# Kernel tuning notes

Hardware: AMD Instinct MI355X
Metric: run time of the kernel (lower is better)

Reference implementation:

```python
import jax, jax.numpy as jnp
import numpy as np

N_NODES = 50000
N_EDGES = 800000
NODE_DIM = 128
IN_CH = 64
OUT_CH = 16
N_GRAPHS = 512
N_LAYERS = 5
BN_EPS = 1e-5


def setup_inputs() -> dict:
    key = jax.random.key(0)
    ks = jax.random.split(key, 16)
    s = lambda fan_in: 1.0 / np.sqrt(fan_in)
    inp = {
        "x": jax.random.normal(ks[0], (N_NODES, NODE_DIM), dtype=jnp.float32),
        "edge_index": jax.random.randint(ks[1], (2, N_EDGES), 0, N_NODES, dtype=jnp.int64),
        "batch": jnp.sort(jax.random.randint(ks[2], (N_NODES,), 0, N_GRAPHS, dtype=jnp.int64)),
        "enc_W": jax.random.normal(ks[3], (NODE_DIM, IN_CH), dtype=jnp.float32) * s(NODE_DIM),
        "enc_b": jnp.zeros((IN_CH,), dtype=jnp.float32),
        "conv_W1": jax.random.normal(ks[4], (N_LAYERS, IN_CH, IN_CH), dtype=jnp.float32) * s(IN_CH),
        "conv_b1": jnp.zeros((N_LAYERS, IN_CH), dtype=jnp.float32),
        "conv_W2": jax.random.normal(ks[5], (N_LAYERS, IN_CH, IN_CH), dtype=jnp.float32) * s(IN_CH),
        "conv_b2": jnp.zeros((N_LAYERS, IN_CH), dtype=jnp.float32),
        "bn_gamma": jnp.ones((N_LAYERS, IN_CH), dtype=jnp.float32),
        "bn_beta": jnp.zeros((N_LAYERS, IN_CH), dtype=jnp.float32),
        "fc1_W": jax.random.normal(ks[6], (IN_CH, IN_CH), dtype=jnp.float32) * s(IN_CH),
        "fc1_b": jnp.zeros((IN_CH,), dtype=jnp.float32),
        "fc2_W": jax.random.normal(ks[7], (IN_CH, OUT_CH), dtype=jnp.float32) * s(IN_CH),
        "fc2_b": jnp.zeros((OUT_CH,), dtype=jnp.float32),
    }
    return inp


def reference(x, edge_index, batch, enc_W, enc_b, conv_W1, conv_b1, conv_W2,
              conv_b2, bn_gamma, bn_beta, fc1_W, fc1_b, fc2_W, fc2_b):
    src, dst = edge_index[0], edge_index[1]
    # node feature encoder
    h = x @ enc_W + enc_b  # [N, C]
    for l in range(N_LAYERS):
        # GINConv (eps=0): (1+eps)*x + sum_{j->i} x_j, then 2-layer MLP
        agg = jax.ops.segment_sum(h[src], dst, num_segments=N_NODES)
        z = h + agg
        z = jax.nn.relu(z @ conv_W1[l] + conv_b1[l]) @ conv_W2[l] + conv_b2[l]
        z = jax.nn.relu(z)
        # BatchNorm1d (training stats, biased variance)
        mean = jnp.mean(z, axis=0)
        var = jnp.mean(jnp.square(z - mean), axis=0)
        h = (z - mean) * jax.lax.rsqrt(var + BN_EPS) * bn_gamma[l] + bn_beta[l]
    # global add pool over graphs
    g = jax.ops.segment_sum(h, batch, num_segments=N_GRAPHS)  # [G, C]
    g = jax.nn.relu(g @ fc1_W + fc1_b)
    # dropout is identity in eval mode
    out = g @ fc2_W + fc2_b  # [G, OUT_CH]
    return out
```

## Files before the change

kernel.cpp:

```cpp
#include <hip/hip_runtime.h>
#include <hip/hip_fp16.h>

#define N_NODES 50000
#define N_EDGES 800000
#define NODE_DIM 128
#define C 64
#define N_GRAPHS 512
#define N_LAYERS 5
#define BN_EPS 1e-5f

#define SCAN_BLOCKS 196
#define NBUCK 196
#define ECHUNK 4096

typedef unsigned int u32;

__device__ inline float2 h2f(u32 v) {
    __half2 h; __builtin_memcpy(&h, &v, 4);
    return __half22float2(h);
}
__device__ inline u32 f2h2(float a, float b) {
    __half2 h = __floats2half2_rn(a, b);
    u32 v; __builtin_memcpy(&v, &h, 4);
    return v;
}

__global__ __launch_bounds__(256) void enc_kernel(const float* __restrict__ x,
                                                  const float* __restrict__ W,
                                                  const float* __restrict__ b,
                                                  u32* __restrict__ z) {
    __shared__ float As[64 * 132];
    __shared__ float Ws[NODE_DIM * C];
    int t = threadIdx.x;
    int tc = t & 15, tr = t >> 4;
    for (int i = t; i < NODE_DIM * C; i += 256) Ws[i] = W[i];
    int row0 = blockIdx.x * 128;
    float4 bv = ((const float4*)b)[tc];
    float acc[8][4];
#pragma unroll
    for (int i = 0; i < 8; ++i) { acc[i][0] = bv.x; acc[i][1] = bv.y; acc[i][2] = bv.z; acc[i][3] = bv.w; }

    for (int kc = 0; kc < 2; ++kc) {
        __syncthreads();
        for (int it = 0; it < 8; ++it) {
            int idx = t + 256 * it;
            int r = idx >> 4, f4 = idx & 15;
            int grow = row0 + r;
            float4 v = (grow < N_NODES) ? ((const float4*)x)[grow * 32 + kc * 16 + f4]
                                        : make_float4(0.f, 0.f, 0.f, 0.f);
            int k4 = f4 * 4;
            As[(k4 + 0) * 132 + r] = v.x;
            As[(k4 + 1) * 132 + r] = v.y;
            As[(k4 + 2) * 132 + r] = v.z;
            As[(k4 + 3) * 132 + r] = v.w;
        }
        __syncthreads();
#pragma unroll 4
        for (int k = 0; k < 64; ++k) {
            const float* ap = As + k * 132 + tr * 8;
            float4 a0 = *(const float4*)(ap);
            float4 a1 = *(const float4*)(ap + 4);
            float4 w = *(const float4*)(Ws + (kc * 64 + k) * C + tc * 4);
            float av[8] = {a0.x, a0.y, a0.z, a0.w, a1.x, a1.y, a1.z, a1.w};
#pragma unroll
            for (int i = 0; i < 8; ++i) {
                acc[i][0] = fmaf(av[i], w.x, acc[i][0]);
                acc[i][1] = fmaf(av[i], w.y, acc[i][1]);
                acc[i][2] = fmaf(av[i], w.z, acc[i][2]);
                acc[i][3] = fmaf(av[i], w.w, acc[i][3]);
            }
        }
    }
#pragma unroll
    for (int i = 0; i < 8; ++i) {
        int grow = row0 + tr * 8 + i;
        if (grow < N_NODES) {
            uint2 o;
            o.x = f2h2(acc[i][0], acc[i][1]);
            o.y = f2h2(acc[i][2], acc[i][3]);
            ((uint2*)z)[grow * 16 + tc] = o;
        }
    }
}

__global__ __launch_bounds__(256) void csr_hist(const int* __restrict__ ei,
                                                int* __restrict__ bcount) {
    __shared__ int lhist[NBUCK];
    int t = threadIdx.x;
    if (t < NBUCK) lhist[t] = 0;
    __syncthreads();
    int e0 = blockIdx.x * ECHUNK;
    int e1 = min(e0 + ECHUNK, N_EDGES);
    for (int e = e0 + t; e < e1; e += 256)
        atomicAdd(&lhist[ei[N_EDGES + e] >> 8], 1);
    __syncthreads();
    if (t < NBUCK && lhist[t] > 0) atomicAdd(&bcount[t], lhist[t]);
}

__global__ __launch_bounds__(256) void csr_bscan(const int* __restrict__ bcount,
                                                 int* __restrict__ bbase,
                                                 int* __restrict__ bcursor,
                                                 int* __restrict__ offs) {
    __shared__ int s[256];
    int t = threadIdx.x;
    int v = (t < NBUCK) ? bcount[t] : 0;
    s[t] = v;
    for (int off = 1; off < 256; off <<= 1) {
        __syncthreads();
        int x = (t >= off) ? s[t - off] : 0;
        __syncthreads();
        s[t] += x;
    }
    __syncthreads();
    if (t < NBUCK) {
        bbase[t + 1] = s[t];
        bcursor[t] = s[t] - v;
    }
    if (t == 0) { bbase[0] = 0; offs[N_NODES] = N_EDGES; }
}

__global__ __launch_bounds__(256) void csr_stage(const int* __restrict__ ei,
                                                 int* __restrict__ bcursor,
                                                 u32* __restrict__ staged) {
    __shared__ int lhist[NBUCK];
    __shared__ int lbase[NBUCK];
    __shared__ int lcur[NBUCK];
    int t = threadIdx.x;
    if (t < NBUCK) lhist[t] = 0;
    __syncthreads();
    int e0 = blockIdx.x * ECHUNK;
    int e1 = min(e0 + ECHUNK, N_EDGES);
    for (int e = e0 + t; e < e1; e += 256)
        atomicAdd(&lhist[ei[N_EDGES + e] >> 8], 1);
    __syncthreads();
    if (t < NBUCK) {
        int c = lhist[t];
        lbase[t] = (c > 0) ? atomicAdd(&bcursor[t], c) : 0;
        lcur[t] = 0;
    }
    __syncthreads();
    for (int e = e0 + t; e < e1; e += 256) {
        int src = ei[e];
        int dst = ei[N_EDGES + e];
        int bk = dst >> 8;
        int r = atomicAdd(&lcur[bk], 1);
        staged[lbase[bk] + r] = (u32)src | ((u32)(dst & 255) << 16);
    }
}

__global__ __launch_bounds__(256) void csr_finalize(const u32* __restrict__ staged,
                                                    const int* __restrict__ bbase,
                                                    int* __restrict__ csr,
                                                    int* __restrict__ offs) {
    __shared__ int lhist[256];
    __shared__ int lexc[256];
    __shared__ int lcur[256];
    int t = threadIdx.x;
    int b = blockIdx.x;
    int sbeg = bbase[b], send = bbase[b + 1];
    lhist[t] = 0;
    __syncthreads();
    for (int i = sbeg + t; i < send; i += 256)
        atomicAdd(&lhist[(staged[i] >> 16) & 255], 1);
    __syncthreads();
    int v = lhist[t];
    lexc[t] = v;
    for (int off = 1; off < 256; off <<= 1) {
        __syncthreads();
        int x = (t >= off) ? lexc[t - off] : 0;
        __syncthreads();
        lexc[t] += x;
    }
    __syncthreads();
    int excl = lexc[t] - v;
    int node = b * 256 + t;
    if (node < N_NODES) offs[node] = sbeg + excl;
    lcur[t] = excl;
    __syncthreads();
    for (int i = sbeg + t; i < send; i += 256) {
        u32 ent = staged[i];
        int dlow = (ent >> 16) & 255;
        int r = atomicAdd(&lcur[dlow], 1);
        csr[sbeg + r] = (int)(ent & 0xFFFFu);
    }
}

__global__ __launch_bounds__(256) void gstart_kernel(const int* __restrict__ batch,
                                                     int* __restrict__ goffs) {
    int n = blockIdx.x * 256 + threadIdx.x;
    if (n >= N_NODES) return;
    if (n == 0) {
        for (int g = 0; g <= batch[0]; ++g) goffs[g] = 0;
    } else {
        int bp = batch[n - 1], bc = batch[n];
        for (int g = bp + 1; g <= bc; ++g) goffs[g] = n;
    }
    if (n == N_NODES - 1) {
        for (int g = batch[n] + 1; g <= N_GRAPHS; ++g) goffs[g] = N_NODES;
    }
}

__global__ __launch_bounds__(256) void mlp_gather_kernel(const int* __restrict__ csr_src,
                                                         const int* __restrict__ offs,
                                                         const u32* __restrict__ z_in,
                                                         const float* __restrict__ ss,
                                                         int use_ss,
                                                         u32* __restrict__ z_out,
                                                         const float* __restrict__ W1,
                                                         const float* __restrict__ b1,
                                                         const float* __restrict__ W2,
                                                         const float* __restrict__ b2,
                                                         float* __restrict__ stats) {
    __shared__ float As[64 * 68];
    __shared__ float Ws[C * C];
    int t = threadIdx.x;
    int tc = t & 15, tr = t >> 4;
    for (int i = t; i < C * C; i += 256) Ws[i] = W1[i];
    int row0 = blockIdx.x * 64;

    float4 sc = make_float4(1.f, 1.f, 1.f, 1.f);
    float4 sh = make_float4(0.f, 0.f, 0.f, 0.f);
    if (use_ss) {
        sc = ((const float4*)ss)[tc];
        sh = ((const float4*)(ss + C))[tc];
    }

    const uint2* z2 = (const uint2*)z_in;
    for (int it = 0; it < 4; ++it) {
        int r = tr + 16 * it;
        int node = row0 + r;
        float4 acc = make_float4(0.f, 0.f, 0.f, 0.f);
        if (node < N_NODES) {
            uint2 sv = z2[node * 16 + tc];
            float2 f0 = h2f(sv.x), f1 = h2f(sv.y);
            acc.x = f0.x; acc.y = f0.y; acc.z = f1.x; acc.w = f1.y;
            int beg = offs[node], end = offs[node + 1];
            int e = beg;
            for (; e + 3 < end; e += 4) {
                int s0 = csr_src[e], s1 = csr_src[e + 1], s2 = csr_src[e + 2], s3 = csr_src[e + 3];
                uint2 v0 = z2[s0 * 16 + tc], v1 = z2[s1 * 16 + tc];
                uint2 v2 = z2[s2 * 16 + tc], v3 = z2[s3 * 16 + tc];
                float2 a0 = h2f(v0.x), a1 = h2f(v1.x), a2 = h2f(v2.x), a3 = h2f(v3.x);
                float2 c0 = h2f(v0.y), c1 = h2f(v1.y), c2 = h2f(v2.y), c3 = h2f(v3.y);
                acc.x += (a0.x + a1.x) + (a2.x + a3.x);
                acc.y += (a0.y + a1.y) + (a2.y + a3.y);
                acc.z += (c0.x + c1.x) + (c2.x + c3.x);
                acc.w += (c0.y + c1.y) + (c2.y + c3.y);
            }
            for (; e < end; ++e) {
                uint2 v = z2[csr_src[e] * 16 + tc];
                float2 a = h2f(v.x), c = h2f(v.y);
                acc.x += a.x; acc.y += a.y; acc.z += c.x; acc.w += c.y;
            }
            float cnt = (float)(end - beg + 1);
            acc.x = fmaf(acc.x, sc.x, cnt * sh.x);
            acc.y = fmaf(acc.y, sc.y, cnt * sh.y);
            acc.z = fmaf(acc.z, sc.z, cnt * sh.z);
            acc.w = fmaf(acc.w, sc.w, cnt * sh.w);
        }
        int k4 = tc * 4;
        As[(k4 + 0) * 68 + r] = acc.x;
        As[(k4 + 1) * 68 + r] = acc.y;
        As[(k4 + 2) * 68 + r] = acc.z;
        As[(k4 + 3) * 68 + r] = acc.w;
    }
    __syncthreads();

    float4 b1v = ((const float4*)b1)[tc];
    float a[4][4];
#pragma unroll
    for (int i = 0; i < 4; ++i) { a[i][0] = b1v.x; a[i][1] = b1v.y; a[i][2] = b1v.z; a[i][3] = b1v.w; }
#pragma unroll 4
    for (int k = 0; k < 64; ++k) {
        float4 av = *(const float4*)(As + k * 68 + tr * 4);
        float4 w = *(const float4*)(Ws + k * C + tc * 4);
        float avv[4] = {av.x, av.y, av.z, av.w};
#pragma unroll
        for (int i = 0; i < 4; ++i) {
            a[i][0] = fmaf(avv[i], w.x, a[i][0]);
            a[i][1] = fmaf(avv[i], w.y, a[i][1]);
            a[i][2] = fmaf(avv[i], w.z, a[i][2]);
            a[i][3] = fmaf(avv[i], w.w, a[i][3]);
        }
    }
    __syncthreads();

#pragma unroll
    for (int i = 0; i < 4; ++i)
#pragma unroll
        for (int j = 0; j < 4; ++j)
            As[(tc * 4 + j) * 68 + tr * 4 + i] = fmaxf(a[i][j], 0.f);
    for (int i = t; i < C * C; i += 256) Ws[i] = W2[i];
    __syncthreads();

    float4 b2v = ((const float4*)b2)[tc];
#pragma unroll
    for (int i = 0; i < 4; ++i) { a[i][0] = b2v.x; a[i][1] = b2v.y; a[i][2] = b2v.z; a[i][3] = b2v.w; }
#pragma unroll 4
    for (int k = 0; k < 64; ++k) {
        float4 av = *(const float4*)(As + k * 68 + tr * 4);
        float4 w = *(const float4*)(Ws + k * C + tc * 4);
        float avv[4] = {av.x, av.y, av.z, av.w};
#pragma unroll
        for (int i = 0; i < 4; ++i) {
            a[i][0] = fmaf(avv[i], w.x, a[i][0]);
            a[i][1] = fmaf(avv[i], w.y, a[i][1]);
            a[i][2] = fmaf(avv[i], w.z, a[i][2]);
            a[i][3] = fmaf(avv[i], w.w, a[i][3]);
        }
    }

    float lsum[4] = {0.f, 0.f, 0.f, 0.f};
    float lsq[4] = {0.f, 0.f, 0.f, 0.f};
#pragma unroll
    for (int i = 0; i < 4; ++i) {
        int grow = row0 + tr * 4 + i;
        if (grow < N_NODES) {
            float o0 = fmaxf(a[i][0], 0.f), o1 = fmaxf(a[i][1], 0.f);
            float o2 = fmaxf(a[i][2], 0.f), o3 = fmaxf(a[i][3], 0.f);
            uint2 o;
            o.x = f2h2(o0, o1);
            o.y = f2h2(o2, o3);
            ((uint2*)z_out)[grow * 16 + tc] = o;
            lsum[0] += o0; lsum[1] += o1; lsum[2] += o2; lsum[3] += o3;
            lsq[0] += o0 * o0; lsq[1] += o1 * o1; lsq[2] += o2 * o2; lsq[3] += o3 * o3;
        }
    }
    __syncthreads();
    float* red = Ws;
#pragma unroll
    for (int j = 0; j < 4; ++j) {
        red[tr * 128 + tc * 4 + j] = lsum[j];
        red[tr * 128 + 64 + tc * 4 + j] = lsq[j];
    }
    __syncthreads();
    if (t < 128) {
        float s = 0.f;
#pragma unroll
        for (int r = 0; r < 16; ++r) s += red[r * 128 + t];
        atomicAdd(&stats[t], s);
    }
}

__global__ void bn_finalize(const float* __restrict__ stats,
                            const float* __restrict__ gamma,
                            const float* __restrict__ beta,
                            float* __restrict__ ss) {
    int c = threadIdx.x;
    if (c >= C) return;
    const float invN = 1.0f / (float)N_NODES;
    float mean = stats[c] * invN;
    float var = stats[C + c] * invN - mean * mean;
    float rstd = rsqrtf(var + BN_EPS);
    float sc = gamma[c] * rstd;
    ss[c] = sc;
    ss[C + c] = beta[c] - mean * sc;
}

__global__ __launch_bounds__(256) void pool_kernel(const u32* __restrict__ z,
                                                   const float* __restrict__ ss,
                                                   const int* __restrict__ goffs,
                                                   float* __restrict__ g) {
    __shared__ float4 red[256];
    int t = threadIdx.x;
    int tc = t & 15, tr = t >> 4;
    int gr = blockIdx.x;
    int beg = goffs[gr], end = goffs[gr + 1];
    const uint2* z2 = (const uint2*)z;
    float4 acc = make_float4(0.f, 0.f, 0.f, 0.f);
    for (int n = beg + tr; n < end; n += 16) {
        uint2 v = z2[n * 16 + tc];
        float2 a = h2f(v.x), c = h2f(v.y);
        acc.x += a.x; acc.y += a.y; acc.z += c.x; acc.w += c.y;
    }
    red[tr * 16 + tc] = acc;
    for (int s = 8; s > 0; s >>= 1) {
        __syncthreads();
        if (tr < s) {
            float4 o = red[(tr + s) * 16 + tc];
            float4 m = red[tr * 16 + tc];
            m.x += o.x; m.y += o.y; m.z += o.z; m.w += o.w;
            red[tr * 16 + tc] = m;
        }
    }
    __syncthreads();
    if (tr == 0) {
        float4 sum = red[tc];
        float4 sc = ((const float4*)ss)[tc];
        float4 sh = ((const float4*)(ss + C))[tc];
        float cnt = (float)(end - beg);
        float4 o;
        o.x = fmaf(sum.x, sc.x, cnt * sh.x);
        o.y = fmaf(sum.y, sc.y, cnt * sh.y);
        o.z = fmaf(sum.z, sc.z, cnt * sh.z);
        o.w = fmaf(sum.w, sc.w, cnt * sh.w);
        ((float4*)g)[gr * 16 + tc] = o;
    }
}

__global__ __launch_bounds__(256) void head_kernel(const float* __restrict__ g,
                                                   const float* __restrict__ fc1W,
                                                   const float* __restrict__ fc1b,
                                                   const float* __restrict__ fc2W,
                                                   const float* __restrict__ fc2b,
                                                   float* __restrict__ out) {
    __shared__ float W1s[C * C];
    __shared__ float W2s[C * 16];
    __shared__ float gs[4][C], t1s[4][C];
    int t = threadIdx.x;
    for (int i = t; i < C * C; i += 256) W1s[i] = fc1W[i];
    for (int i = t; i < C * 16; i += 256) W2s[i] = fc2W[i];
    int ch = t & 63, rr = t >> 6;
    int g0 = blockIdx.x * 4;
    gs[rr][ch] = g[(g0 + rr) * C + ch];
    __syncthreads();
    float a1 = fc1b[ch];
#pragma unroll 8
    for (int k = 0; k < C; ++k) a1 = fmaf(gs[rr][k], W1s[k * C + ch], a1);
    t1s[rr][ch] = fmaxf(a1, 0.f);
    __syncthreads();
    if (t < 64) {
        int o = t & 15, r2 = t >> 4;
        float a2 = fc2b[o];
#pragma unroll 8
        for (int k = 0; k < C; ++k) a2 = fmaf(t1s[r2][k], W2s[k * 16 + o], a2);
        out[(g0 + r2) * 16 + o] = a2;
    }
}

extern "C" void kernel_launch(void* const* d_in, const int* in_sizes, int n_in,
                              void* d_out, int out_size, void* d_ws, size_t ws_size,
                              hipStream_t stream) {
    const float* x    = (const float*)d_in[0];
    const int*   ei   = (const int*)d_in[1];
    const int*   batch= (const int*)d_in[2];
    const float* encW = (const float*)d_in[3];
    const float* encb = (const float*)d_in[4];
    const float* cW1  = (const float*)d_in[5];
    const float* cb1  = (const float*)d_in[6];
    const float* cW2  = (const float*)d_in[7];
    const float* cb2  = (const float*)d_in[8];
    const float* gam  = (const float*)d_in[9];
    const float* bet  = (const float*)d_in[10];
    const float* f1W  = (const float*)d_in[11];
    const float* f1b  = (const float*)d_in[12];
    const float* f2W  = (const float*)d_in[13];
    const float* f2b  = (const float*)d_in[14];
    float* out = (float*)d_out;

    char* ws = (char*)d_ws;
    u32*   zA      = (u32*)  (ws);
    u32*   zB      = (u32*)  (ws + 6400000);
    int*   csr     = (int*)  (ws + 12800000);
    u32*   staged  = (u32*)  (ws + 16000000);
    int*   offs    = (int*)  (ws + 19200000);
    int*   bcount  = (int*)  (ws + 19400064);
    int*   bbase   = (int*)  (ws + 19401088);
    int*   bcursor = (int*)  (ws + 19402112);
    float* stats   = (float*)(ws + 19403136);
    float* ssb     = (float*)(ws + 19405696);
    int*   goffs   = (int*)  (ws + 19408256);
    float* gpool   = (float*)(ws + 19410432);

    hipMemsetAsync(bcount, 0, NBUCK * sizeof(int), stream);
    hipMemsetAsync(stats, 0, 5 * 2 * C * sizeof(float), stream);
    csr_hist<<<NBUCK, 256, 0, stream>>>(ei, bcount);
    csr_bscan<<<1, 256, 0, stream>>>(bcount, bbase, bcursor, offs);
    csr_stage<<<NBUCK, 256, 0, stream>>>(ei, bcursor, staged);
    csr_finalize<<<NBUCK, 256, 0, stream>>>(staged, bbase, csr, offs);
    gstart_kernel<<<SCAN_BLOCKS, 256, 0, stream>>>(batch, goffs);

    enc_kernel<<<(N_NODES + 127) / 128, 256, 0, stream>>>(x, encW, encb, zA);

    u32* zin = zA;
    u32* zout = zB;
    for (int l = 0; l < N_LAYERS; ++l) {
        const float* ss_prev = (l > 0) ? (ssb + (size_t)(l - 1) * 2 * C) : ssb;
        mlp_gather_kernel<<<(N_NODES + 63) / 64, 256, 0, stream>>>(
            csr, offs, zin, ss_prev, l > 0 ? 1 : 0, zout,
            cW1 + (size_t)l * C * C, cb1 + (size_t)l * C,
            cW2 + (size_t)l * C * C, cb2 + (size_t)l * C,
            stats + (size_t)l * 2 * C);
        bn_finalize<<<1, 64, 0, stream>>>(stats + (size_t)l * 2 * C,
                                          gam + (size_t)l * C, bet + (size_t)l * C,
                                          ssb + (size_t)l * 2 * C);
        u32* tmp = zin; zin = zout; zout = tmp;
    }

    pool_kernel<<<N_GRAPHS, 256, 0, stream>>>(zin, ssb + (size_t)(N_LAYERS - 1) * 2 * C, goffs, gpool);
    head_kernel<<<N_GRAPHS / 4, 256, 0, stream>>>(gpool, f1W, f1b, f2W, f2b, out);
}
```

Baseline: 433.0 us.

## Use 16-bit CSR indices, 16-byte gather loads, and fp16 shared staging

Stores CSR source indices as u16, which is valid because node ids are below 65536, halving index traffic in the gather. The gather now uses 8 threads per row, each loading 16-byte uint4 chunks of fp16 features, which means fewer, wider memory requests per edge. The aggregated and hidden activations are staged in shared memory as packed fp16 instead of fp32, halving LDS footprint and read traffic in both 64x64 matmuls. The cost is extra fp16 rounding of the aggregated sums before the MLP, which adds precision risk, and fewer threads working on each row.

```diff
diff --git a/kernel.cpp b/kernel.cpp
--- a/kernel.cpp
+++ b/kernel.cpp
@@ -14,6 +14,7 @@
 #define ECHUNK 4096
 
 typedef unsigned int u32;
+typedef unsigned short u16;
 
 __device__ inline float2 h2f(u32 v) {
     __half2 h; __builtin_memcpy(&h, &v, 4);
@@ -150,7 +151,7 @@
 
 __global__ __launch_bounds__(256) void csr_finalize(const u32* __restrict__ staged,
                                                     const int* __restrict__ bbase,
-                                                    int* __restrict__ csr,
+                                                    u16* __restrict__ csr,
                                                     int* __restrict__ offs) {
     __shared__ int lhist[256];
     __shared__ int lexc[256];
@@ -181,7 +182,7 @@
         u32 ent = staged[i];
         int dlow = (ent >> 16) & 255;
         int r = atomicAdd(&lcur[dlow], 1);
-        csr[sbeg + r] = (int)(ent & 0xFFFFu);
+        csr[sbeg + r] = (u16)(ent & 0xFFFFu);
     }
 }
 
@@ -200,7 +201,7 @@
     }
 }
 
-__global__ __launch_bounds__(256) void mlp_gather_kernel(const int* __restrict__ csr_src,
+__global__ __launch_bounds__(256) void mlp_gather_kernel(const u16* __restrict__ csr_src,
                                                          const int* __restrict__ offs,
                                                          const u32* __restrict__ z_in,
                                                          const float* __restrict__ ss,
@@ -211,58 +212,73 @@
                                                          const float* __restrict__ W2,
                                                          const float* __restrict__ b2,
                                                          float* __restrict__ stats) {
-    __shared__ float As[64 * 68];
+    __shared__ u32 Asw[32 * 68];
     __shared__ float Ws[C * C];
     int t = threadIdx.x;
     int tc = t & 15, tr = t >> 4;
     for (int i = t; i < C * C; i += 256) Ws[i] = W1[i];
     int row0 = blockIdx.x * 64;
 
-    float4 sc = make_float4(1.f, 1.f, 1.f, 1.f);
-    float4 sh = make_float4(0.f, 0.f, 0.f, 0.f);
+    int tg = t & 7;
+    int rg = t >> 3;
+    float scv[8], shv[8];
     if (use_ss) {
-        sc = ((const float4*)ss)[tc];
-        sh = ((const float4*)(ss + C))[tc];
-    }
-
-    const uint2* z2 = (const uint2*)z_in;
-    for (int it = 0; it < 4; ++it) {
-        int r = tr + 16 * it;
+        float4 s0 = ((const float4*)ss)[tg * 2], s1 = ((const float4*)ss)[tg * 2 + 1];
+        float4 h0 = ((const float4*)(ss + C))[tg * 2], h1 = ((const float4*)(ss + C))[tg * 2 + 1];
+        scv[0] = s0.x; scv[1] = s0.y; scv[2] = s0.z; scv[3] = s0.w;
+        scv[4] = s1.x; scv[5] = s1.y; scv[6] = s1.z; scv[7] = s1.w;
+        shv[0] = h0.x; shv[1] = h0.y; shv[2] = h0.z; shv[3] = h0.w;
+        shv[4] = h1.x; shv[5] = h1.y; shv[6] = h1.z; shv[7] = h1.w;
+    } else {
+#pragma unroll
+        for (int i = 0; i < 8; ++i) { scv[i] = 1.f; shv[i] = 0.f; }
+    }
+    const uint4* z4 = (const uint4*)z_in;
+#pragma unroll
+    for (int it = 0; it < 2; ++it) {
+        int r = rg + 32 * it;
         int node = row0 + r;
-        float4 acc = make_float4(0.f, 0.f, 0.f, 0.f);
+        float acc[8] = {0.f, 0.f, 0.f, 0.f, 0.f, 0.f, 0.f, 0.f};
         if (node < N_NODES) {
-            uint2 sv = z2[node * 16 + tc];
-            float2 f0 = h2f(sv.x), f1 = h2f(sv.y);
-            acc.x = f0.x; acc.y = f0.y; acc.z = f1.x; acc.w = f1.y;
+            uint4 sv = z4[node * 8 + tg];
+            {
+                float2 p0 = h2f(sv.x), p1 = h2f(sv.y), p2 = h2f(sv.z), p3 = h2f(sv.w);
+                acc[0] = p0.x; acc[1] = p0.y; acc[2] = p1.x; acc[3] = p1.y;
+                acc[4] = p2.x; acc[5] = p2.y; acc[6] = p3.x; acc[7] = p3.y;
+            }
             int beg = offs[node], end = offs[node + 1];
             int e = beg;
             for (; e + 3 < end; e += 4) {
                 int s0 = csr_src[e], s1 = csr_src[e + 1], s2 = csr_src[e + 2], s3 = csr_src[e + 3];
-                uint2 v0 = z2[s0 * 16 + tc], v1 = z2[s1 * 16 + tc];
-                uint2 v2 = z2[s2 * 16 + tc], v3 = z2[s3 * 16 + tc];
+                uint4 v0 = z4[s0 * 8 + tg], v1 = z4[s1 * 8 + tg];
+                uint4 v2 = z4[s2 * 8 + tg], v3 = z4[s3 * 8 + tg];
                 float2 a0 = h2f(v0.x), a1 = h2f(v1.x), a2 = h2f(v2.x), a3 = h2f(v3.x);
-                float2 c0 = h2f(v0.y), c1 = h2f(v1.y), c2 = h2f(v2.y), c3 = h2f(v3.y);
-                acc.x += (a0.x + a1.x) + (a2.x + a3.x);
-                acc.y += (a0.y + a1.y) + (a2.y + a3.y);
-                acc.z += (c0.x + c1.x) + (c2.x + c3.x);
-                acc.w += (c0.y + c1.y) + (c2.y + c3.y);
+                acc[0] += (a0.x + a1.x) + (a2.x + a3.x);
+                acc[1] += (a0.y + a1.y) + (a2.y + a3.y);
+                a0 = h2f(v0.y); a1 = h2f(v1.y); a2 = h2f(v2.y); a3 = h2f(v3.y);
+                acc[2] += (a0.x + a1.x) + (a2.x + a3.x);
+                acc[3] += (a0.y + a1.y) + (a2.y + a3.y);
+                a0 = h2f(v0.z); a1 = h2f(v1.z); a2 = h2f(v2.z); a3 = h2f(v3.z);
+                acc[4] += (a0.x + a1.x) + (a2.x + a3.x);
+                acc[5] += (a0.y + a1.y) + (a2.y + a3.y);
+                a0 = h2f(v0.w); a1 = h2f(v1.w); a2 = h2f(v2.w); a3 = h2f(v3.w);
+                acc[6] += (a0.x + a1.x) + (a2.x + a3.x);
+                acc[7] += (a0.y + a1.y) + (a2.y + a3.y);
             }
             for (; e < end; ++e) {
-                uint2 v = z2[csr_src[e] * 16 + tc];
-                float2 a = h2f(v.x), c = h2f(v.y);
-                acc.x += a.x; acc.y += a.y; acc.z += c.x; acc.w += c.y;
+                uint4 v = z4[csr_src[e] * 8 + tg];
+                float2 a0 = h2f(v.x), a1 = h2f(v.y), a2 = h2f(v.z), a3 = h2f(v.w);
+                acc[0] += a0.x; acc[1] += a0.y; acc[2] += a1.x; acc[3] += a1.y;
+                acc[4] += a2.x; acc[5] += a2.y; acc[6] += a3.x; acc[7] += a3.y;
             }
             float cnt = (float)(end - beg + 1);
-            acc.x = fmaf(acc.x, sc.x, cnt * sh.x);
-            acc.y = fmaf(acc.y, sc.y, cnt * sh.y);
-            acc.z = fmaf(acc.z, sc.z, cnt * sh.z);
-            acc.w = fmaf(acc.w, sc.w, cnt * sh.w);
-        }
-        int k4 = tc * 4;
-        As[(k4 + 0) * 68 + r] = acc.x;
-        As[(k4 + 1) * 68 + r] = acc.y;
-        As[(k4 + 2) * 68 + r] = acc.z;
-        As[(k4 + 3) * 68 + r] = acc.w;
+#pragma unroll
+            for (int i = 0; i < 8; ++i) acc[i] = fmaf(acc[i], scv[i], cnt * shv[i]);
+        }
+        Asw[(tg * 4 + 0) * 68 + r] = f2h2(acc[0], acc[1]);
+        Asw[(tg * 4 + 1) * 68 + r] = f2h2(acc[2], acc[3]);
+        Asw[(tg * 4 + 2) * 68 + r] = f2h2(acc[4], acc[5]);
+        Asw[(tg * 4 + 3) * 68 + r] = f2h2(acc[6], acc[7]);
     }
     __syncthreads();
 
@@ -270,43 +286,57 @@
     float a[4][4];
 #pragma unroll
     for (int i = 0; i < 4; ++i) { a[i][0] = b1v.x; a[i][1] = b1v.y; a[i][2] = b1v.z; a[i][3] = b1v.w; }
-#pragma unroll 4
-    for (int k = 0; k < 64; ++k) {
-        float4 av = *(const float4*)(As + k * 68 + tr * 4);
-        float4 w = *(const float4*)(Ws + k * C + tc * 4);
-        float avv[4] = {av.x, av.y, av.z, av.w};
+#pragma unroll 2
+    for (int w = 0; w < 32; ++w) {
+        uint4 aw = *(const uint4*)(Asw + w * 68 + tr * 4);
+        float2 r0 = h2f(aw.x), r1 = h2f(aw.y), r2 = h2f(aw.z), r3 = h2f(aw.w);
+        float4 w0 = *(const float4*)(Ws + (2 * w) * C + tc * 4);
+        float4 w1 = *(const float4*)(Ws + (2 * w + 1) * C + tc * 4);
+        float e0[4] = {r0.x, r1.x, r2.x, r3.x};
+        float e1[4] = {r0.y, r1.y, r2.y, r3.y};
 #pragma unroll
         for (int i = 0; i < 4; ++i) {
-            a[i][0] = fmaf(avv[i], w.x, a[i][0]);
-            a[i][1] = fmaf(avv[i], w.y, a[i][1]);
-            a[i][2] = fmaf(avv[i], w.z, a[i][2]);
-            a[i][3] = fmaf(avv[i], w.w, a[i][3]);
-        }
-    }
-    __syncthreads();
-
-#pragma unroll
-    for (int i = 0; i < 4; ++i)
-#pragma unroll
-        for (int j = 0; j < 4; ++j)
-            As[(tc * 4 + j) * 68 + tr * 4 + i] = fmaxf(a[i][j], 0.f);
+            a[i][0] = fmaf(e0[i], w0.x, a[i][0]); a[i][0] = fmaf(e1[i], w1.x, a[i][0]);
+            a[i][1] = fmaf(e0[i], w0.y, a[i][1]); a[i][1] = fmaf(e1[i], w1.y, a[i][1]);
+            a[i][2] = fmaf(e0[i], w0.z, a[i][2]); a[i][2] = fmaf(e1[i], w1.z, a[i][2]);
+            a[i][3] = fmaf(e0[i], w0.w, a[i][3]); a[i][3] = fmaf(e1[i], w1.w, a[i][3]);
+        }
+    }
+    __syncthreads();
+
+    {
+        uint4 w0, w1;
+        w0.x = f2h2(fmaxf(a[0][0], 0.f), fmaxf(a[0][1], 0.f));
+        w0.y = f2h2(fmaxf(a[1][0], 0.f), fmaxf(a[1][1], 0.f));
+        w0.z = f2h2(fmaxf(a[2][0], 0.f), fmaxf(a[2][1], 0.f));
+        w0.w = f2h2(fmaxf(a[3][0], 0.f), fmaxf(a[3][1], 0.f));
+        w1.x = f2h2(fmaxf(a[0][2], 0.f), fmaxf(a[0][3], 0.f));
+        w1.y = f2h2(fmaxf(a[1][2], 0.f), fmaxf(a[1][3], 0.f));
+        w1.z = f2h2(fmaxf(a[2][2], 0.f), fmaxf(a[2][3], 0.f));
+        w1.w = f2h2(fmaxf(a[3][2], 0.f), fmaxf(a[3][3], 0.f));
+        *(uint4*)(Asw + (tc * 2) * 68 + tr * 4) = w0;
+        *(uint4*)(Asw + (tc * 2 + 1) * 68 + tr * 4) = w1;
+    }
     for (int i = t; i < C * C; i += 256) Ws[i] = W2[i];
     __syncthreads();
 
     float4 b2v = ((const float4*)b2)[tc];
 #pragma unroll
     for (int i = 0; i < 4; ++i) { a[i][0] = b2v.x; a[i][1] = b2v.y; a[i][2] = b2v.z; a[i][3] = b2v.w; }
-#pragma unroll 4
-    for (int k = 0; k < 64; ++k) {
-        float4 av = *(const float4*)(As + k * 68 + tr * 4);
-        float4 w = *(const float4*)(Ws + k * C + tc * 4);
-        float avv[4] = {av.x, av.y, av.z, av.w};
+#pragma unroll 2
+    for (int w = 0; w < 32; ++w) {
+        uint4 aw = *(const uint4*)(Asw + w * 68 + tr * 4);
+        float2 r0 = h2f(aw.x), r1 = h2f(aw.y), r2 = h2f(aw.z), r3 = h2f(aw.w);
+        float4 w0 = *(const float4*)(Ws + (2 * w) * C + tc * 4);
+        float4 w1 = *(const float4*)(Ws + (2 * w + 1) * C + tc * 4);
+        float e0[4] = {r0.x, r1.x, r2.x, r3.x};
+        float e1[4] = {r0.y, r1.y, r2.y, r3.y};
 #pragma unroll
         for (int i = 0; i < 4; ++i) {
-            a[i][0] = fmaf(avv[i], w.x, a[i][0]);
-            a[i][1] = fmaf(avv[i], w.y, a[i][1]);
-            a[i][2] = fmaf(avv[i], w.z, a[i][2]);
-            a[i][3] = fmaf(avv[i], w.w, a[i][3]);
+            a[i][0] = fmaf(e0[i], w0.x, a[i][0]); a[i][0] = fmaf(e1[i], w1.x, a[i][0]);
+            a[i][1] = fmaf(e0[i], w0.y, a[i][1]); a[i][1] = fmaf(e1[i], w1.y, a[i][1]);
+            a[i][2] = fmaf(e0[i], w0.z, a[i][2]); a[i][2] = fmaf(e1[i], w1.z, a[i][2]);
+            a[i][3] = fmaf(e0[i], w0.w, a[i][3]); a[i][3] = fmaf(e1[i], w1.w, a[i][3]);
         }
     }
 
@@ -451,7 +481,7 @@
     char* ws = (char*)d_ws;
     u32*   zA      = (u32*)  (ws);
     u32*   zB      = (u32*)  (ws + 6400000);
-    int*   csr     = (int*)  (ws + 12800000);
+    u16*   csr     = (u16*)  (ws + 12800000);
     u32*   staged  = (u32*)  (ws + 16000000);
     int*   offs    = (int*)  (ws + 19200000);
     int*   bcount  = (int*)  (ws + 19400064);
```

Measured after the change: 393.1 us. 9.2% less time.
